# Performance work log

Hardware: AMD Instinct MI355X
Metric: run time of the kernel (lower is better)

The kernel has to match this reference:

```python
import jax, jax.numpy as jnp
import numpy as np

B, S, D = 8, 2048, 512
MINF = 20000.0  # matches tf code's -20000.0 mask constant


def setup_inputs() -> dict:
    key = jax.random.key(0)
    k1, k2, k3 = jax.random.split(key, 3)
    x1 = jax.random.normal(k1, (B, S, D), dtype=jnp.float32)
    x2 = jax.random.normal(k2, (B, S, D), dtype=jnp.float32)
    # glorot_normal init for the learned (S, S) positional kernel
    std = np.sqrt(2.0 / (S + S)).astype(np.float32)
    kernel = jax.random.normal(k3, (S, S), dtype=jnp.float32) * std
    return {"x1": x1, "x2": x2, "kernel": kernel}


def reference(x1, x2, kernel):
    S_ = kernel.shape[0]
    # tf.matmul(kernel, inputs[i]) broadcasts (S,S) @ (B,S,D) -> (B,S,D)
    h1 = jnp.einsum('st,btd->bsd', kernel, x1)
    h2 = jnp.einsum('st,btd->bsd', kernel, x2)
    # att_scores: (B, S, S)
    scores = jnp.einsum('bsd,btd->bst', h1, h2)
    d_k = jnp.asarray(S_, dtype=scores.dtype) ** 0.5
    # upper_m[i,j] = -20000 for j > i (strictly upper), else 0; added BEFORE scaling
    row = jnp.arange(S_)
    mask = jnp.where(row[None, :] > row[:, None], -MINF, 0.0).astype(scores.dtype)
    attn = jax.nn.softmax((scores + mask) / d_k, axis=-1)
    # note: output attends over h1 (not h2), as in the original code
    return jnp.einsum('bst,btd->bsd', attn, h1)
```

## Files before the change

kernel.cpp:

```cpp
#include <hip/hip_runtime.h>
#include <hip/hip_bf16.h>

#define S_DIM 2048
#define D_DIM 512
#define B_DIM 8
#define SCALE 0.02209708691207961f

typedef __hip_bfloat16 bf16;
typedef short bf16x8 __attribute__((ext_vector_type(8)));
typedef float f32x4 __attribute__((ext_vector_type(4)));

__device__ __forceinline__ unsigned short f2b(float f) {
  __hip_bfloat16 h = __float2bfloat16(f);
  return __builtin_bit_cast(unsigned short, h);
}
__device__ __forceinline__ float b2f(unsigned short s) {
  return __bfloat162float(__builtin_bit_cast(__hip_bfloat16, s));
}

__device__ __forceinline__ void load_lds16(const void* g, void* l) {
  __builtin_amdgcn_global_load_lds((const __attribute__((address_space(1))) void*)g,
                                   (__attribute__((address_space(3))) void*)l, 16, 0, 0);
}

__global__ void convert_k(const float* __restrict__ in, bf16* __restrict__ out, int n8) {
  int i = blockIdx.x * blockDim.x + threadIdx.x;
  if (i >= n8) return;
  const float4* p = (const float4*)in;
  float4 a = p[2 * i], b = p[2 * i + 1];
  bf16x8 r;
  r[0] = f2b(a.x); r[1] = f2b(a.y); r[2] = f2b(a.z); r[3] = f2b(a.w);
  r[4] = f2b(b.x); r[5] = f2b(b.y); r[6] = f2b(b.z); r[7] = f2b(b.w);
  ((bf16x8*)out)[i] = r;
}

__global__ void transpose_f2b(const float* __restrict__ in, bf16* __restrict__ out) {
  __shared__ float tile[32][33];
  int b = blockIdx.z;
  int c0 = blockIdx.x * 32;
  int r0 = blockIdx.y * 32;
  const float* ib = in + (size_t)b * S_DIM * D_DIM;
  bf16* ob = out + (size_t)b * S_DIM * D_DIM;
  int lr = threadIdx.x >> 5, lc = threadIdx.x & 31;
#pragma unroll
  for (int i = 0; i < 4; i++)
    tile[lr + i * 8][lc] = ib[(size_t)(r0 + lr + i * 8) * D_DIM + c0 + lc];
  __syncthreads();
#pragma unroll
  for (int i = 0; i < 4; i++) {
    int cc = lr + i * 8;
    ob[(size_t)(c0 + cc) * S_DIM + r0 + lc] = __float2bfloat16(tile[lc][cc]);
  }
}

__global__ void transpose_b2b(const bf16* __restrict__ in, bf16* __restrict__ out) {
  __shared__ bf16 tile[32][33];
  int b = blockIdx.z;
  int c0 = blockIdx.x * 32;
  int r0 = blockIdx.y * 32;
  const bf16* ib = in + (size_t)b * S_DIM * D_DIM;
  bf16* ob = out + (size_t)b * S_DIM * D_DIM;
  int lr = threadIdx.x >> 5, lc = threadIdx.x & 31;
#pragma unroll
  for (int i = 0; i < 4; i++)
    tile[lr + i * 8][lc] = ib[(size_t)(r0 + lr + i * 8) * D_DIM + c0 + lc];
  __syncthreads();
#pragma unroll
  for (int i = 0; i < 4; i++) {
    int cc = lr + i * 8;
    ob[(size_t)(c0 + cc) * S_DIM + r0 + lc] = tile[lc][cc];
  }
}

__global__ __launch_bounds__(512, 2) void gemm_h(
    const bf16* __restrict__ A, const bf16* __restrict__ X, bf16* __restrict__ H) {
  extern __shared__ char smem[];
  const int pid = blockIdx.x;
  const int mt = pid & 7;
  const int r_ = pid >> 3;
  const int ntile = r_ & 1;
  const int item = r_ >> 1;
  const int m0 = mt * 256, n0 = ntile * 256;
  const bf16* Xi = X + (size_t)item * (D_DIM * S_DIM);
  bf16* Hi = H + (size_t)item * (S_DIM * D_DIM);

  const int tid = threadIdx.x;
  const int w = tid >> 6, L = tid & 63;
  const int l15 = L & 15, lhi = L >> 4;
  const int wr = w >> 2, wn = w & 3;

  const int srow = tid >> 2;
  const int sslot = ((tid & 3) ^ ((tid >> 3) & 3)) * 8;
  const bf16* pA[2];
  const bf16* pB[2];
#pragma unroll
  for (int ld = 0; ld < 2; ld++) {
    pA[ld] = A + (size_t)(m0 + ld * 128 + srow) * 2048 + sslot;
    pB[ld] = Xi + (size_t)(n0 + ld * 128 + srow) * 2048 + sslot;
  }

  char* A0 = smem;          char* A1 = smem + 16384;  char* A2 = smem + 32768;
  char* B0 = smem + 49152;  char* B1 = smem + 65536;  char* B2 = smem + 81920;

  auto stage = [&](int t2, char* dA, char* dB) {
#pragma unroll
    for (int ld = 0; ld < 2; ld++)
      load_lds16(pA[ld] + t2 * 32, dA + ld * 8192 + w * 1024);
#pragma unroll
    for (int ld = 0; ld < 2; ld++)
      load_lds16(pB[ld] + t2 * 32, dB + ld * 8192 + w * 1024);
  };

  const int xo = (lhi ^ ((l15 >> 1) & 3)) << 4;
  int offA[8], offB[4];
#pragma unroll
  for (int m = 0; m < 8; m++) offA[m] = (wr * 128 + m * 16 + l15) * 64 + xo;
#pragma unroll
  for (int n = 0; n < 4; n++) offB[n] = (wn * 64 + n * 16 + l15) * 64 + xo;

  f32x4 acc[8][4];
#pragma unroll
  for (int m = 0; m < 8; m++)
#pragma unroll
    for (int n = 0; n < 4; n++) acc[m][n] = (f32x4){0, 0, 0, 0};

  stage(0, A0, B0);
  stage(1, A1, B1);

#pragma unroll 1
  for (int t = 0; t < 64; ++t) {
    if (t < 63) asm volatile("s_waitcnt vmcnt(4)" ::: "memory");
    else        asm volatile("s_waitcnt vmcnt(0)" ::: "memory");
    __builtin_amdgcn_s_barrier();
    asm volatile("" ::: "memory");
    if (t < 62) stage(t + 2, A2, B2);

    bf16x8 af[8], bfv[4];
#pragma unroll
    for (int m = 0; m < 8; m++) af[m] = *(const bf16x8*)(A0 + offA[m]);
#pragma unroll
    for (int n = 0; n < 4; n++) bfv[n] = *(const bf16x8*)(B0 + offB[n]);
    __builtin_amdgcn_s_setprio(1);
#pragma unroll
    for (int m = 0; m < 8; m++)
#pragma unroll
      for (int n = 0; n < 4; n++)
        acc[m][n] = __builtin_amdgcn_mfma_f32_16x16x32_bf16(bfv[n], af[m], acc[m][n], 0, 0, 0);
    __builtin_amdgcn_s_setprio(0);

    char* tA = A0; A0 = A1; A1 = A2; A2 = tA;
    char* tB = B0; B0 = B1; B1 = B2; B2 = tB;
  }

#pragma unroll
  for (int m = 0; m < 8; m++) {
    int grow = m0 + wr * 128 + m * 16 + l15;
#pragma unroll
    for (int n = 0; n < 4; n++) {
      int gcol = n0 + wn * 64 + n * 16 + lhi * 4;
      uint2 u;
      u.x = ((unsigned)f2b(acc[m][n][1]) << 16) | f2b(acc[m][n][0]);
      u.y = ((unsigned)f2b(acc[m][n][3]) << 16) | f2b(acc[m][n][2]);
      *(uint2*)(Hi + (size_t)grow * D_DIM + gcol) = u;
    }
  }
}

__global__ __launch_bounds__(512, 2) void gemm_score(
    const bf16* __restrict__ H1, const bf16* __restrict__ H2,
    bf16* __restrict__ E, float* __restrict__ rowsum) {
  extern __shared__ char smem[];
  const int pid = blockIdx.x;
  const int b = pid & 7;
  const int tri = pid >> 3;
  int mt = (int)((sqrtf(8.0f * (float)tri + 1.0f) - 1.0f) * 0.5f);
  while ((mt + 1) * (mt + 2) / 2 <= tri) mt++;
  while (mt * (mt + 1) / 2 > tri) mt--;
  const int nt = tri - mt * (mt + 1) / 2;
  const int m0 = mt * 256, n0 = nt * 256;
  const bool diag = (mt == nt);
  const bf16* Ab = H1 + (size_t)b * S_DIM * D_DIM;
  const bf16* Bb = H2 + (size_t)b * S_DIM * D_DIM;
  bf16* Eb = E + (size_t)b * S_DIM * S_DIM;
  float* rs = rowsum + b * S_DIM;

  const int tid = threadIdx.x;
  const int w = tid >> 6, L = tid & 63;
  const int l15 = L & 15, lhi = L >> 4;
  const int wr = w >> 2, wn = w & 3;

  const int srow = tid >> 2;
  const int sslot = ((tid & 3) ^ ((tid >> 3) & 3)) * 8;
  const bf16* pA[2];
  const bf16* pB[2];
#pragma unroll
  for (int ld = 0; ld < 2; ld++) {
    pA[ld] = Ab + (size_t)(m0 + ld * 128 + srow) * D_DIM + sslot;
    pB[ld] = Bb + (size_t)(n0 + ld * 128 + srow) * D_DIM + sslot;
  }

  char* A0 = smem;          char* A1 = smem + 16384;  char* A2 = smem + 32768;
  char* B0 = smem + 49152;  char* B1 = smem + 65536;  char* B2 = smem + 81920;

  auto stage = [&](int t2, char* dA, char* dB) {
#pragma unroll
    for (int ld = 0; ld < 2; ld++)
      load_lds16(pA[ld] + t2 * 32, dA + ld * 8192 + w * 1024);
#pragma unroll
    for (int ld = 0; ld < 2; ld++)
      load_lds16(pB[ld] + t2 * 32, dB + ld * 8192 + w * 1024);
  };

  const int xo = (lhi ^ ((l15 >> 1) & 3)) << 4;
  int offA[8], offB[4];
#pragma unroll
  for (int m = 0; m < 8; m++) offA[m] = (wr * 128 + m * 16 + l15) * 64 + xo;
#pragma unroll
  for (int n = 0; n < 4; n++) offB[n] = (wn * 64 + n * 16 + l15) * 64 + xo;

  f32x4 acc[8][4];
#pragma unroll
  for (int m = 0; m < 8; m++)
#pragma unroll
    for (int n = 0; n < 4; n++) acc[m][n] = (f32x4){0, 0, 0, 0};

  stage(0, A0, B0);
  stage(1, A1, B1);

#pragma unroll 1
  for (int t = 0; t < 16; ++t) {
    if (t < 15) asm volatile("s_waitcnt vmcnt(4)" ::: "memory");
    else        asm volatile("s_waitcnt vmcnt(0)" ::: "memory");
    __builtin_amdgcn_s_barrier();
    asm volatile("" ::: "memory");
    if (t < 14) stage(t + 2, A2, B2);

    bf16x8 af[8], bfv[4];
#pragma unroll
    for (int m = 0; m < 8; m++) af[m] = *(const bf16x8*)(A0 + offA[m]);
#pragma unroll
    for (int n = 0; n < 4; n++) bfv[n] = *(const bf16x8*)(B0 + offB[n]);
    __builtin_amdgcn_s_setprio(1);
#pragma unroll
    for (int m = 0; m < 8; m++)
#pragma unroll
      for (int n = 0; n < 4; n++)
        acc[m][n] = __builtin_amdgcn_mfma_f32_16x16x32_bf16(bfv[n], af[m], acc[m][n], 0, 0, 0);
    __builtin_amdgcn_s_setprio(0);

    char* tA = A0; A0 = A1; A1 = A2; A2 = tA;
    char* tB = B0; B0 = B1; B1 = B2; B2 = tB;
  }

#pragma unroll
  for (int m = 0; m < 8; m++) {
    int sg = m0 + wr * 128 + m * 16 + l15;
    float rp = 0.0f;
#pragma unroll
    for (int n = 0; n < 4; n++) {
      int tg0 = n0 + wn * 64 + n * 16 + lhi * 4;
      unsigned short e[4];
#pragma unroll
      for (int r = 0; r < 4; r++) {
        float v = (!diag || (tg0 + r) <= sg) ? __expf(acc[m][n][r] * SCALE) : 0.0f;
        e[r] = f2b(v);
        rp += b2f(e[r]);
      }
      uint2 u;
      u.x = ((unsigned)e[1] << 16) | e[0];
      u.y = ((unsigned)e[3] << 16) | e[2];
      *(uint2*)(Eb + (size_t)sg * S_DIM + tg0) = u;
    }
    rp += __shfl_xor(rp, 16);
    rp += __shfl_xor(rp, 32);
    if (lhi == 0) atomicAdd(rs + sg, rp);
  }
}

__global__ __launch_bounds__(256, 2) void gemm_pv(
    const bf16* __restrict__ E, const bf16* __restrict__ H1T,
    const float* __restrict__ rowsum, float* __restrict__ out) {
  __shared__ bf16 As[128][32];
  __shared__ bf16 Bs[128][32];
  int pid = blockIdx.x;
  int b = pid & 7;
  int r_ = pid >> 3;
  int nt = r_ & 3;
  int mb = r_ >> 2;
  int mt = (mb < 8) ? 2 * mb : 31 - 2 * mb;
  int m0 = mt * 128, n0 = nt * 128;
  int KMAX = (mt + 1) * 128;
  const bf16* Ab = E + (size_t)b * S_DIM * S_DIM;
  const bf16* Bb = H1T + (size_t)b * D_DIM * S_DIM;
  const float* rs = rowsum + b * S_DIM;
  float* Cb = out + (size_t)b * S_DIM * D_DIM;
  int tid = threadIdx.x, wave = tid >> 6, lane = tid & 63;
  int wr = wave >> 1, wc = wave & 1;
  int srow = lane >> 2;
  int skh = (lane & 3) * 8;
  int l15 = lane & 15, lhi = lane >> 4;
  int lk = lhi * 8;
  f32x4 acc[4][4];
#pragma unroll
  for (int m = 0; m < 4; m++)
#pragma unroll
    for (int n = 0; n < 4; n++) acc[m][n] = (f32x4){0, 0, 0, 0};

  for (int k0 = 0; k0 < KMAX; k0 += 32) {
#pragma unroll
    for (int c = 0; c < 2; c++) {
      int chunk = wave * 2 + c;
      int row = chunk * 16 + srow;
      load_lds16(Ab + (size_t)(m0 + row) * S_DIM + k0 + skh, (char*)&As[0][0] + chunk * 1024);
      load_lds16(Bb + (size_t)(n0 + row) * S_DIM + k0 + skh, (char*)&Bs[0][0] + chunk * 1024);
    }
    __syncthreads();
    bf16x8 af[4], bfr[4];
#pragma unroll
    for (int m = 0; m < 4; m++) af[m] = *(const bf16x8*)&As[wr * 64 + m * 16 + l15][lk];
#pragma unroll
    for (int n = 0; n < 4; n++) bfr[n] = *(const bf16x8*)&Bs[wc * 64 + n * 16 + l15][lk];
#pragma unroll
    for (int m = 0; m < 4; m++)
#pragma unroll
      for (int n = 0; n < 4; n++)
        acc[m][n] = __builtin_amdgcn_mfma_f32_16x16x32_bf16(af[m], bfr[n], acc[m][n], 0, 0, 0);
    __syncthreads();
  }
#pragma unroll
  for (int m = 0; m < 4; m++) {
#pragma unroll
    for (int r = 0; r < 4; r++) {
      int sg = m0 + wr * 64 + m * 16 + lhi * 4 + r;
      float inv = 1.0f / rs[sg];
#pragma unroll
      for (int n = 0; n < 4; n++) {
        int gcol = n0 + wc * 64 + n * 16 + l15;
        Cb[(size_t)sg * D_DIM + gcol] = acc[m][n][r] * inv;
      }
    }
  }
}

extern "C" void kernel_launch(void* const* d_in, const int* in_sizes, int n_in,
                              void* d_out, int out_size, void* d_ws, size_t ws_size,
                              hipStream_t stream) {
  const float* x1 = (const float*)d_in[0];
  const float* x2 = (const float*)d_in[1];
  const float* km = (const float*)d_in[2];
  float* out = (float*)d_out;
  char* ws = (char*)d_ws;
  bf16* E    = (bf16*)(ws);
  bf16* Kbf  = (bf16*)(ws);
  bf16* x1t  = (bf16*)(ws + (8ull << 20));
  bf16* x2t  = (bf16*)(ws + (24ull << 20));
  bf16* h1n  = (bf16*)(ws + (64ull << 20));
  bf16* h2n  = (bf16*)(ws + (80ull << 20));
  bf16* h1t  = (bf16*)(ws + (96ull << 20));
  float* rowsum = (float*)(ws + (112ull << 20));

  convert_k<<<2048, 256, 0, stream>>>(km, Kbf, (S_DIM * S_DIM) / 8);
  transpose_f2b<<<dim3(16, 64, 8), 256, 0, stream>>>(x1, x1t);
  transpose_f2b<<<dim3(16, 64, 8), 256, 0, stream>>>(x2, x2t);
  gemm_h<<<256, 512, 98304, stream>>>(Kbf, x1t, h1n);
  transpose_b2b<<<dim3(16, 64, 8), 256, 0, stream>>>(h1n, h1t);
  hipMemsetAsync(rowsum, 0, B_DIM * S_DIM * sizeof(float), stream);
  gemm_score<<<288, 512, 98304, stream>>>(h1n, h2n, E, rowsum);
  gemm_pv<<<512, 256, 0, stream>>>(E, h1t, rowsum, out);
}
```

Baseline: 190.8 us.

## Share a BK=64 double-buffered GEMM core with quarter-step load/MFMA interleave

Factors the two 256x256 bf16 MFMA GEMMs (the positional-kernel projection and the attention-score GEMM) into one templated core. The core uses a K-tile of 64 with 8-way XOR swizzled LDS and double buffering in 128 KB of shared memory. Each K-tile is split into four quadrant MFMA phases separated by barriers, with the next tile's A and B global-to-LDS loads issued between phases. The goal is to hide global load latency behind MFMA work and cut the number of outer-loop barriers per unit of K. The cost is more barriers within each tile and a larger LDS footprint, which could limit occupancy or add synchronisation stalls.

```diff
diff --git a/kernel.cpp b/kernel.cpp
--- a/kernel.cpp
+++ b/kernel.cpp
@@ -72,6 +72,119 @@
   }
 }
 
+template <int NT, int LDE>
+__device__ __forceinline__ void gemm_core256(
+    const bf16* __restrict__ Asrc, const bf16* __restrict__ Bsrc,
+    char* smem, f32x4 (*acc)[4]) {
+  const int tid = threadIdx.x;
+  const int w = tid >> 6, L = tid & 63;
+  const int l15 = L & 15, lhi = L >> 4;
+  const int wr = w >> 2, wn = w & 3;
+
+  const int srow = w * 16 + (L >> 3);
+  const int sslot = ((L & 7) ^ (L >> 3)) * 8;
+  const bf16* pA[2][2];
+  const bf16* pB[2][2];
+#pragma unroll
+  for (int h = 0; h < 2; h++)
+#pragma unroll
+    for (int ld = 0; ld < 2; ld++) {
+      pA[h][ld] = Asrc + (size_t)(h * 128 + srow + ld * 8) * LDE + sslot;
+      pB[h][ld] = Bsrc + (size_t)(h * 128 + srow + ld * 8) * LDE + sslot;
+    }
+
+  auto stageA = [&](int t2, int half) {
+    char* d = smem + (((t2 & 1) * 2 + half) << 14) + w * 2048;
+    const int ko = t2 * 64;
+#pragma unroll
+    for (int ld = 0; ld < 2; ld++)
+      load_lds16(pA[half][ld] + ko, d + ld * 1024);
+  };
+  auto stageB = [&](int t2, int half) {
+    char* d = smem + 65536 + (((t2 & 1) * 2 + half) << 14) + w * 2048;
+    const int ko = t2 * 64;
+#pragma unroll
+    for (int ld = 0; ld < 2; ld++)
+      load_lds16(pB[half][ld] + ko, d + ld * 1024);
+  };
+
+  const int xsw = l15 & 7;
+  const int cK0 = ((0 + lhi) ^ xsw) << 4;
+  const int cK1 = ((4 + lhi) ^ xsw) << 4;
+  const int rowA = l15 * 128;
+  const int rowB = ((wn & 1) * 64 + l15) * 128;
+
+  bf16x8 af0[4][2], af1[4][2], bfr[2][2];
+  auto readA = [&](int buf, int mh, bf16x8 (&af)[4][2]) {
+    const char* base = smem + ((buf * 2 + wr) << 14) + mh * 8192 + rowA;
+#pragma unroll
+    for (int m = 0; m < 4; m++) {
+      af[m][0] = *(const bf16x8*)(base + m * 2048 + cK0);
+      af[m][1] = *(const bf16x8*)(base + m * 2048 + cK1);
+    }
+  };
+  auto readB = [&](int buf, int nh) {
+    const char* base = smem + 65536 + ((buf * 2 + (wn >> 1)) << 14) + nh * 2048 * 2 + rowB;
+#pragma unroll
+    for (int n = 0; n < 2; n++) {
+      bfr[n][0] = *(const bf16x8*)(base + n * 2048 + cK0);
+      bfr[n][1] = *(const bf16x8*)(base + n * 2048 + cK1);
+    }
+  };
+  auto mfmaQ = [&](int mh, int nh, bf16x8 (&af)[4][2]) {
+    __builtin_amdgcn_s_setprio(1);
+#pragma unroll
+    for (int kk = 0; kk < 2; kk++)
+#pragma unroll
+      for (int m = 0; m < 4; m++)
+#pragma unroll
+        for (int n = 0; n < 2; n++)
+          acc[mh * 4 + m][nh * 2 + n] = __builtin_amdgcn_mfma_f32_16x16x32_bf16(
+              bfr[n][kk], af[m][kk], acc[mh * 4 + m][nh * 2 + n], 0, 0, 0);
+    __builtin_amdgcn_s_setprio(0);
+  };
+  auto midsync = [&] {
+    __builtin_amdgcn_s_barrier();
+    asm volatile("s_waitcnt lgkmcnt(0)" ::: "memory");
+    __builtin_amdgcn_sched_barrier(0);
+  };
+  auto endbar = [&] {
+    __builtin_amdgcn_s_barrier();
+    asm volatile("" ::: "memory");
+  };
+
+  stageA(0, 0); stageA(0, 1); stageB(0, 0); stageB(0, 1);
+  stageA(1, 0); stageA(1, 1);
+  asm volatile("s_waitcnt vmcnt(4)" ::: "memory");
+  __builtin_amdgcn_s_barrier();
+  asm volatile("" ::: "memory");
+
+  auto ktile = [&](int t, int buf) {
+    const bool sB = (t + 1 < NT);
+    const bool sA = (t + 2 < NT);
+    readA(buf, 0, af0); readB(buf, 0);
+    if (sB) stageB(t + 1, 0);
+    midsync(); mfmaQ(0, 0, af0); endbar();
+    readA(buf, 1, af1);
+    if (sB) stageB(t + 1, 1);
+    midsync(); mfmaQ(1, 0, af1); endbar();
+    readB(buf, 1);
+    if (sA) stageA(t + 2, 0);
+    midsync(); mfmaQ(1, 1, af1); endbar();
+    if (sA) stageA(t + 2, 1);
+    midsync(); mfmaQ(0, 1, af0);
+    if (sA) asm volatile("s_waitcnt vmcnt(4)" ::: "memory");
+    else    asm volatile("s_waitcnt vmcnt(0)" ::: "memory");
+    endbar();
+  };
+
+#pragma unroll 1
+  for (int t = 0; t < NT; t += 2) {
+    ktile(t, 0);
+    ktile(t + 1, 1);
+  }
+}
+
 __global__ __launch_bounds__(512, 2) void gemm_h(
     const bf16* __restrict__ A, const bf16* __restrict__ X, bf16* __restrict__ H) {
   extern __shared__ char smem[];
@@ -81,77 +194,22 @@
   const int ntile = r_ & 1;
   const int item = r_ >> 1;
   const int m0 = mt * 256, n0 = ntile * 256;
-  const bf16* Xi = X + (size_t)item * (D_DIM * S_DIM);
+  const bf16* Asrc = A + (size_t)m0 * S_DIM;
+  const bf16* Bsrc = X + (size_t)item * (D_DIM * S_DIM) + (size_t)n0 * S_DIM;
   bf16* Hi = H + (size_t)item * (S_DIM * D_DIM);
+
+  f32x4 acc[8][4];
+#pragma unroll
+  for (int m = 0; m < 8; m++)
+#pragma unroll
+    for (int n = 0; n < 4; n++) acc[m][n] = (f32x4){0, 0, 0, 0};
+
+  gemm_core256<32, S_DIM>(Asrc, Bsrc, smem, acc);
 
   const int tid = threadIdx.x;
   const int w = tid >> 6, L = tid & 63;
   const int l15 = L & 15, lhi = L >> 4;
   const int wr = w >> 2, wn = w & 3;
-
-  const int srow = tid >> 2;
-  const int sslot = ((tid & 3) ^ ((tid >> 3) & 3)) * 8;
-  const bf16* pA[2];
-  const bf16* pB[2];
-#pragma unroll
-  for (int ld = 0; ld < 2; ld++) {
-    pA[ld] = A + (size_t)(m0 + ld * 128 + srow) * 2048 + sslot;
-    pB[ld] = Xi + (size_t)(n0 + ld * 128 + srow) * 2048 + sslot;
-  }
-
-  char* A0 = smem;          char* A1 = smem + 16384;  char* A2 = smem + 32768;
-  char* B0 = smem + 49152;  char* B1 = smem + 65536;  char* B2 = smem + 81920;
-
-  auto stage = [&](int t2, char* dA, char* dB) {
-#pragma unroll
-    for (int ld = 0; ld < 2; ld++)
-      load_lds16(pA[ld] + t2 * 32, dA + ld * 8192 + w * 1024);
-#pragma unroll
-    for (int ld = 0; ld < 2; ld++)
-      load_lds16(pB[ld] + t2 * 32, dB + ld * 8192 + w * 1024);
-  };
-
-  const int xo = (lhi ^ ((l15 >> 1) & 3)) << 4;
-  int offA[8], offB[4];
-#pragma unroll
-  for (int m = 0; m < 8; m++) offA[m] = (wr * 128 + m * 16 + l15) * 64 + xo;
-#pragma unroll
-  for (int n = 0; n < 4; n++) offB[n] = (wn * 64 + n * 16 + l15) * 64 + xo;
-
-  f32x4 acc[8][4];
-#pragma unroll
-  for (int m = 0; m < 8; m++)
-#pragma unroll
-    for (int n = 0; n < 4; n++) acc[m][n] = (f32x4){0, 0, 0, 0};
-
-  stage(0, A0, B0);
-  stage(1, A1, B1);
-
-#pragma unroll 1
-  for (int t = 0; t < 64; ++t) {
-    if (t < 63) asm volatile("s_waitcnt vmcnt(4)" ::: "memory");
-    else        asm volatile("s_waitcnt vmcnt(0)" ::: "memory");
-    __builtin_amdgcn_s_barrier();
-    asm volatile("" ::: "memory");
-    if (t < 62) stage(t + 2, A2, B2);
-
-    bf16x8 af[8], bfv[4];
-#pragma unroll
-    for (int m = 0; m < 8; m++) af[m] = *(const bf16x8*)(A0 + offA[m]);
-#pragma unroll
-    for (int n = 0; n < 4; n++) bfv[n] = *(const bf16x8*)(B0 + offB[n]);
-    __builtin_amdgcn_s_setprio(1);
-#pragma unroll
-    for (int m = 0; m < 8; m++)
-#pragma unroll
-      for (int n = 0; n < 4; n++)
-        acc[m][n] = __builtin_amdgcn_mfma_f32_16x16x32_bf16(bfv[n], af[m], acc[m][n], 0, 0, 0);
-    __builtin_amdgcn_s_setprio(0);
-
-    char* tA = A0; A0 = A1; A1 = A2; A2 = tA;
-    char* tB = B0; B0 = B1; B1 = B2; B2 = tB;
-  }
-
 #pragma unroll
   for (int m = 0; m < 8; m++) {
     int grow = m0 + wr * 128 + m * 16 + l15;
@@ -184,74 +242,18 @@
   bf16* Eb = E + (size_t)b * S_DIM * S_DIM;
   float* rs = rowsum + b * S_DIM;
 
+  f32x4 acc[8][4];
+#pragma unroll
+  for (int m = 0; m < 8; m++)
+#pragma unroll
+    for (int n = 0; n < 4; n++) acc[m][n] = (f32x4){0, 0, 0, 0};
+
+  gemm_core256<8, D_DIM>(Ab + (size_t)m0 * D_DIM, Bb + (size_t)n0 * D_DIM, smem, acc);
+
   const int tid = threadIdx.x;
   const int w = tid >> 6, L = tid & 63;
   const int l15 = L & 15, lhi = L >> 4;
   const int wr = w >> 2, wn = w & 3;
-
-  const int srow = tid >> 2;
-  const int sslot = ((tid & 3) ^ ((tid >> 3) & 3)) * 8;
-  const bf16* pA[2];
-  const bf16* pB[2];
-#pragma unroll
-  for (int ld = 0; ld < 2; ld++) {
-    pA[ld] = Ab + (size_t)(m0 + ld * 128 + srow) * D_DIM + sslot;
-    pB[ld] = Bb + (size_t)(n0 + ld * 128 + srow) * D_DIM + sslot;
-  }
-
-  char* A0 = smem;          char* A1 = smem + 16384;  char* A2 = smem + 32768;
-  char* B0 = smem + 49152;  char* B1 = smem + 65536;  char* B2 = smem + 81920;
-
-  auto stage = [&](int t2, char* dA, char* dB) {
-#pragma unroll
-    for (int ld = 0; ld < 2; ld++)
-      load_lds16(pA[ld] + t2 * 32, dA + ld * 8192 + w * 1024);
-#pragma unroll
-    for (int ld = 0; ld < 2; ld++)
-      load_lds16(pB[ld] + t2 * 32, dB + ld * 8192 + w * 1024);
-  };
-
-  const int xo = (lhi ^ ((l15 >> 1) & 3)) << 4;
-  int offA[8], offB[4];
-#pragma unroll
-  for (int m = 0; m < 8; m++) offA[m] = (wr * 128 + m * 16 + l15) * 64 + xo;
-#pragma unroll
-  for (int n = 0; n < 4; n++) offB[n] = (wn * 64 + n * 16 + l15) * 64 + xo;
-
-  f32x4 acc[8][4];
-#pragma unroll
-  for (int m = 0; m < 8; m++)
-#pragma unroll
-    for (int n = 0; n < 4; n++) acc[m][n] = (f32x4){0, 0, 0, 0};
-
-  stage(0, A0, B0);
-  stage(1, A1, B1);
-
-#pragma unroll 1
-  for (int t = 0; t < 16; ++t) {
-    if (t < 15) asm volatile("s_waitcnt vmcnt(4)" ::: "memory");
-    else        asm volatile("s_waitcnt vmcnt(0)" ::: "memory");
-    __builtin_amdgcn_s_barrier();
-    asm volatile("" ::: "memory");
-    if (t < 14) stage(t + 2, A2, B2);
-
-    bf16x8 af[8], bfv[4];
-#pragma unroll
-    for (int m = 0; m < 8; m++) af[m] = *(const bf16x8*)(A0 + offA[m]);
-#pragma unroll
-    for (int n = 0; n < 4; n++) bfv[n] = *(const bf16x8*)(B0 + offB[n]);
-    __builtin_amdgcn_s_setprio(1);
-#pragma unroll
-    for (int m = 0; m < 8; m++)
-#pragma unroll
-      for (int n = 0; n < 4; n++)
-        acc[m][n] = __builtin_amdgcn_mfma_f32_16x16x32_bf16(bfv[n], af[m], acc[m][n], 0, 0, 0);
-    __builtin_amdgcn_s_setprio(0);
-
-    char* tA = A0; A0 = A1; A1 = A2; A2 = tA;
-    char* tB = B0; B0 = B1; B1 = B2; B2 = tB;
-  }
-
 #pragma unroll
   for (int m = 0; m < 8; m++) {
     int sg = m0 + wr * 128 + m * 16 + l15;
@@ -362,9 +364,9 @@
   convert_k<<<2048, 256, 0, stream>>>(km, Kbf, (S_DIM * S_DIM) / 8);
   transpose_f2b<<<dim3(16, 64, 8), 256, 0, stream>>>(x1, x1t);
   transpose_f2b<<<dim3(16, 64, 8), 256, 0, stream>>>(x2, x2t);
-  gemm_h<<<256, 512, 98304, stream>>>(Kbf, x1t, h1n);
+  gemm_h<<<256, 512, 131072, stream>>>(Kbf, x1t, h1n);
   transpose_b2b<<<dim3(16, 64, 8), 256, 0, stream>>>(h1n, h1t);
   hipMemsetAsync(rowsum, 0, B_DIM * S_DIM * sizeof(float), stream);
-  gemm_score<<<288, 512, 98304, stream>>>(h1n, h2n, E, rowsum);
+  gemm_score<<<288, 512, 131072, stream>>>(h1n, h2n, E, rowsum);
   gemm_pv<<<512, 256, 0, stream>>>(E, h1t, rowsum, out);
 }
```

Measured after the change: 218.5 us. 14.5% more time.

## Triple-buffer gemm_pv with swizzled LDS and widen transpose kernels

Applied to the files above, without the earlier changes.

gemm_pv is rewritten with a three-stage LDS ring buffer using async global-to-LDS loads, waitcnt-based sync instead of two full barriers per step, an XOR swizzle to avoid bank conflicts, swapped MFMA operands, and float4 output stores. The transposes move to 64x64 tiles with packed 8-byte stores, and the two input transposes are merged into one launch covering both x1 and x2 (z=16). The x2 transpose now writes contiguously after x1t instead of at a separate offset, so gemm_h's indexing of items 8-15 must match this layout. The design relies on the vmcnt counts matching the number of in-flight loads.

```diff
diff --git a/kernel.cpp b/kernel.cpp
--- a/kernel.cpp
+++ b/kernel.cpp
@@ -34,41 +34,60 @@
   ((bf16x8*)out)[i] = r;
 }
 
-__global__ void transpose_f2b(const float* __restrict__ in, bf16* __restrict__ out) {
-  __shared__ float tile[32][33];
-  int b = blockIdx.z;
-  int c0 = blockIdx.x * 32;
-  int r0 = blockIdx.y * 32;
-  const float* ib = in + (size_t)b * S_DIM * D_DIM;
-  bf16* ob = out + (size_t)b * S_DIM * D_DIM;
-  int lr = threadIdx.x >> 5, lc = threadIdx.x & 31;
-#pragma unroll
-  for (int i = 0; i < 4; i++)
-    tile[lr + i * 8][lc] = ib[(size_t)(r0 + lr + i * 8) * D_DIM + c0 + lc];
+__global__ void tr_f2b64(const float* __restrict__ x1, const float* __restrict__ x2,
+                         bf16* __restrict__ out) {
+  __shared__ unsigned short t[64][66];
+  const int z = blockIdx.z;
+  const float* in = (z < 8 ? x1 : x2) + (size_t)(z & 7) * (S_DIM * D_DIM);
+  bf16* ob = out + (size_t)z * (size_t)(D_DIM * S_DIM);
+  const int r0 = blockIdx.y * 64;
+  const int c0 = blockIdx.x * 64;
+  const int tid = threadIdx.x;
+  const int lr = tid >> 6, lc = tid & 63;
+#pragma unroll
+  for (int i = 0; i < 16; i++) {
+    int r = i * 4 + lr;
+    t[lc][r] = f2b(in[(size_t)(r0 + r) * D_DIM + c0 + lc]);
+  }
   __syncthreads();
-#pragma unroll
-  for (int i = 0; i < 4; i++) {
-    int cc = lr + i * 8;
-    ob[(size_t)(c0 + cc) * S_DIM + r0 + lc] = __float2bfloat16(tile[lc][cc]);
-  }
-}
-
-__global__ void transpose_b2b(const bf16* __restrict__ in, bf16* __restrict__ out) {
-  __shared__ bf16 tile[32][33];
-  int b = blockIdx.z;
-  int c0 = blockIdx.x * 32;
-  int r0 = blockIdx.y * 32;
-  const bf16* ib = in + (size_t)b * S_DIM * D_DIM;
-  bf16* ob = out + (size_t)b * S_DIM * D_DIM;
-  int lr = threadIdx.x >> 5, lc = threadIdx.x & 31;
-#pragma unroll
-  for (int i = 0; i < 4; i++)
-    tile[lr + i * 8][lc] = ib[(size_t)(r0 + lr + i * 8) * D_DIM + c0 + lc];
+  const int dl = tid >> 4, tq = tid & 15;
+#pragma unroll
+  for (int j = 0; j < 4; j++) {
+    int d = j * 16 + dl;
+    const unsigned short* p = &t[d][tq * 4];
+    uint2 u;
+    u.x = (unsigned)p[0] | ((unsigned)p[1] << 16);
+    u.y = (unsigned)p[2] | ((unsigned)p[3] << 16);
+    *(uint2*)(ob + (size_t)(c0 + d) * S_DIM + r0 + tq * 4) = u;
+  }
+}
+
+__global__ void tr_b2b64(const bf16* __restrict__ in, bf16* __restrict__ out) {
+  __shared__ unsigned short t[64][66];
+  const int z = blockIdx.z;
+  const bf16* ib = in + (size_t)z * (S_DIM * D_DIM);
+  bf16* ob = out + (size_t)z * (S_DIM * D_DIM);
+  const int r0 = blockIdx.y * 64;
+  const int c0 = blockIdx.x * 64;
+  const int tid = threadIdx.x;
+  const int lr = tid >> 5, cp = tid & 31;
+#pragma unroll
+  for (int i = 0; i < 8; i++) {
+    int r = i * 8 + lr;
+    unsigned v = *(const unsigned*)(ib + (size_t)(r0 + r) * D_DIM + c0 + cp * 2);
+    t[cp * 2][r] = (unsigned short)(v & 0xffff);
+    t[cp * 2 + 1][r] = (unsigned short)(v >> 16);
+  }
   __syncthreads();
-#pragma unroll
-  for (int i = 0; i < 4; i++) {
-    int cc = lr + i * 8;
-    ob[(size_t)(c0 + cc) * S_DIM + r0 + lc] = tile[lc][cc];
+  const int dl = tid >> 4, tq = tid & 15;
+#pragma unroll
+  for (int j = 0; j < 4; j++) {
+    int d = j * 16 + dl;
+    const unsigned short* p = &t[d][tq * 4];
+    uint2 u;
+    u.x = (unsigned)p[0] | ((unsigned)p[1] << 16);
+    u.y = (unsigned)p[2] | ((unsigned)p[3] << 16);
+    *(uint2*)(ob + (size_t)(c0 + d) * S_DIM + r0 + tq * 4) = u;
   }
 }
 
@@ -280,64 +299,101 @@
 __global__ __launch_bounds__(256, 2) void gemm_pv(
     const bf16* __restrict__ E, const bf16* __restrict__ H1T,
     const float* __restrict__ rowsum, float* __restrict__ out) {
-  __shared__ bf16 As[128][32];
-  __shared__ bf16 Bs[128][32];
-  int pid = blockIdx.x;
-  int b = pid & 7;
-  int r_ = pid >> 3;
-  int nt = r_ & 3;
-  int mb = r_ >> 2;
-  int mt = (mb < 8) ? 2 * mb : 31 - 2 * mb;
-  int m0 = mt * 128, n0 = nt * 128;
-  int KMAX = (mt + 1) * 128;
-  const bf16* Ab = E + (size_t)b * S_DIM * S_DIM;
-  const bf16* Bb = H1T + (size_t)b * D_DIM * S_DIM;
+  extern __shared__ char smem[];
+  const int pid = blockIdx.x;
+  const int b = pid & 7;
+  const int r_ = pid >> 3;
+  const int nt = r_ & 3;
+  const int mb = r_ >> 2;
+  const int mt = (mb < 8) ? 2 * mb : 31 - 2 * mb;
+  const int m0 = mt * 128, n0 = nt * 128;
+  const int NT = (mt + 1) * 4;
+  const bf16* Ab = E + (size_t)b * S_DIM * S_DIM + (size_t)m0 * S_DIM;
+  const bf16* Bb = H1T + (size_t)b * D_DIM * S_DIM + (size_t)n0 * S_DIM;
   const float* rs = rowsum + b * S_DIM;
   float* Cb = out + (size_t)b * S_DIM * D_DIM;
-  int tid = threadIdx.x, wave = tid >> 6, lane = tid & 63;
-  int wr = wave >> 1, wc = wave & 1;
-  int srow = lane >> 2;
-  int skh = (lane & 3) * 8;
-  int l15 = lane & 15, lhi = lane >> 4;
-  int lk = lhi * 8;
+
+  const int tid = threadIdx.x;
+  const int w = tid >> 6, L = tid & 63;
+  const int l15 = L & 15, lhi = L >> 4;
+  const int wr = w >> 1, wc = w & 1;
+
+  const int srow = tid >> 2;
+  const int sslot = ((tid & 3) ^ ((tid >> 3) & 3)) * 8;
+  const bf16* pA[2];
+  const bf16* pB[2];
+#pragma unroll
+  for (int ld = 0; ld < 2; ld++) {
+    pA[ld] = Ab + (size_t)(ld * 64 + srow) * S_DIM + sslot;
+    pB[ld] = Bb + (size_t)(ld * 64 + srow) * S_DIM + sslot;
+  }
+
+  char* A0 = smem;          char* A1 = smem + 8192;   char* A2 = smem + 16384;
+  char* B0 = smem + 24576;  char* B1 = smem + 32768;  char* B2 = smem + 40960;
+
+  auto stage = [&](int t2, char* dA, char* dB) {
+#pragma unroll
+    for (int ld = 0; ld < 2; ld++)
+      load_lds16(pA[ld] + t2 * 32, dA + ld * 4096 + w * 1024);
+#pragma unroll
+    for (int ld = 0; ld < 2; ld++)
+      load_lds16(pB[ld] + t2 * 32, dB + ld * 4096 + w * 1024);
+  };
+
+  const int xo = (lhi ^ ((l15 >> 1) & 3)) << 4;
+  int offA[4], offB[4];
+#pragma unroll
+  for (int m = 0; m < 4; m++) offA[m] = (wr * 64 + m * 16 + l15) * 64 + xo;
+#pragma unroll
+  for (int n = 0; n < 4; n++) offB[n] = (wc * 64 + n * 16 + l15) * 64 + xo;
+
   f32x4 acc[4][4];
 #pragma unroll
   for (int m = 0; m < 4; m++)
 #pragma unroll
     for (int n = 0; n < 4; n++) acc[m][n] = (f32x4){0, 0, 0, 0};
 
-  for (int k0 = 0; k0 < KMAX; k0 += 32) {
-#pragma unroll
-    for (int c = 0; c < 2; c++) {
-      int chunk = wave * 2 + c;
-      int row = chunk * 16 + srow;
-      load_lds16(Ab + (size_t)(m0 + row) * S_DIM + k0 + skh, (char*)&As[0][0] + chunk * 1024);
-      load_lds16(Bb + (size_t)(n0 + row) * S_DIM + k0 + skh, (char*)&Bs[0][0] + chunk * 1024);
-    }
-    __syncthreads();
-    bf16x8 af[4], bfr[4];
-#pragma unroll
-    for (int m = 0; m < 4; m++) af[m] = *(const bf16x8*)&As[wr * 64 + m * 16 + l15][lk];
-#pragma unroll
-    for (int n = 0; n < 4; n++) bfr[n] = *(const bf16x8*)&Bs[wc * 64 + n * 16 + l15][lk];
+  stage(0, A0, B0);
+  stage(1, A1, B1);
+
+#pragma unroll 1
+  for (int t = 0; t < NT; ++t) {
+    if (t < NT - 1) asm volatile("s_waitcnt vmcnt(4)" ::: "memory");
+    else            asm volatile("s_waitcnt vmcnt(0)" ::: "memory");
+    __builtin_amdgcn_s_barrier();
+    asm volatile("" ::: "memory");
+    if (t + 2 < NT) stage(t + 2, A2, B2);
+
+    bf16x8 af[4], bfv[4];
+#pragma unroll
+    for (int m = 0; m < 4; m++) af[m] = *(const bf16x8*)(A0 + offA[m]);
+#pragma unroll
+    for (int n = 0; n < 4; n++) bfv[n] = *(const bf16x8*)(B0 + offB[n]);
+    __builtin_amdgcn_s_setprio(1);
 #pragma unroll
     for (int m = 0; m < 4; m++)
 #pragma unroll
       for (int n = 0; n < 4; n++)
-        acc[m][n] = __builtin_amdgcn_mfma_f32_16x16x32_bf16(af[m], bfr[n], acc[m][n], 0, 0, 0);
-    __syncthreads();
-  }
+        acc[m][n] = __builtin_amdgcn_mfma_f32_16x16x32_bf16(bfv[n], af[m], acc[m][n], 0, 0, 0);
+    __builtin_amdgcn_s_setprio(0);
+
+    char* tA = A0; A0 = A1; A1 = A2; A2 = tA;
+    char* tB = B0; B0 = B1; B1 = B2; B2 = tB;
+  }
+
 #pragma unroll
   for (int m = 0; m < 4; m++) {
-#pragma unroll
-    for (int r = 0; r < 4; r++) {
-      int sg = m0 + wr * 64 + m * 16 + lhi * 4 + r;
-      float inv = 1.0f / rs[sg];
-#pragma unroll
-      for (int n = 0; n < 4; n++) {
-        int gcol = n0 + wc * 64 + n * 16 + l15;
-        Cb[(size_t)sg * D_DIM + gcol] = acc[m][n][r] * inv;
-      }
+    int sg = m0 + wr * 64 + m * 16 + l15;
+    float inv = 1.0f / rs[sg];
+#pragma unroll
+    for (int n = 0; n < 4; n++) {
+      int gcol = n0 + wc * 64 + n * 16 + lhi * 4;
+      float4 o;
+      o.x = acc[m][n][0] * inv;
+      o.y = acc[m][n][1] * inv;
+      o.z = acc[m][n][2] * inv;
+      o.w = acc[m][n][3] * inv;
+      *(float4*)(Cb + (size_t)sg * D_DIM + gcol) = o;
     }
   }
 }
@@ -353,18 +409,16 @@
   bf16* E    = (bf16*)(ws);
   bf16* Kbf  = (bf16*)(ws);
   bf16* x1t  = (bf16*)(ws + (8ull << 20));
-  bf16* x2t  = (bf16*)(ws + (24ull << 20));
   bf16* h1n  = (bf16*)(ws + (64ull << 20));
   bf16* h2n  = (bf16*)(ws + (80ull << 20));
   bf16* h1t  = (bf16*)(ws + (96ull << 20));
   float* rowsum = (float*)(ws + (112ull << 20));
 
   convert_k<<<2048, 256, 0, stream>>>(km, Kbf, (S_DIM * S_DIM) / 8);
-  transpose_f2b<<<dim3(16, 64, 8), 256, 0, stream>>>(x1, x1t);
-  transpose_f2b<<<dim3(16, 64, 8), 256, 0, stream>>>(x2, x2t);
+  tr_f2b64<<<dim3(8, 32, 16), 256, 0, stream>>>(x1, x2, x1t);
   gemm_h<<<256, 512, 98304, stream>>>(Kbf, x1t, h1n);
-  transpose_b2b<<<dim3(16, 64, 8), 256, 0, stream>>>(h1n, h1t);
+  tr_b2b64<<<dim3(8, 32, 8), 256, 0, stream>>>(h1n, h1t);
   hipMemsetAsync(rowsum, 0, B_DIM * S_DIM * sizeof(float), stream);
   gemm_score<<<288, 512, 98304, stream>>>(h1n, h2n, E, rowsum);
-  gemm_pv<<<512, 256, 0, stream>>>(E, h1t, rowsum, out);
-}
+  gemm_pv<<<512, 256, 49152, stream>>>(E, h1t, rowsum, out);
+}
```

Measured after the change: 173.9 us. 8.9% less time.
